# Performance work log

Measured on AMD Instinct MI355X. Metric: run time of the kernel, lower is better.

## Reference

```python
import jax, jax.numpy as jnp
import numpy as np

TOPK = 9
ALPHA = 0.25
GAMMA = 2.0


def setup_inputs() -> dict:
    key = jax.random.key(0)
    ks = jax.random.split(key, 5)
    B, N, C, G = 16, 21504, 80, 64
    return {
        "pred_logits": jax.random.normal(ks[0], (B, N, C), dtype=jnp.float32),
        "pred_boxes": jax.random.uniform(ks[1], (B, N, 4), dtype=jnp.float32),
        "locations": jax.random.uniform(ks[2], (N, 2), dtype=jnp.float32),
        "gt_boxes": jax.random.uniform(ks[3], (B, G, 4), dtype=jnp.float32),
        "gt_labels": jax.random.randint(ks[4], (B, G), 0, C),
    }


def _cxcywh_to_xyxy(b):
    c, wh = b[..., :2], b[..., 2:]
    return jnp.concatenate([c - 0.5 * wh, c + 0.5 * wh], axis=-1)


def _giou_pairwise(a, b):
    # elementwise GIoU between matched xyxy boxes [..., 4] -> [...]
    area_a = (a[..., 2] - a[..., 0]) * (a[..., 3] - a[..., 1])
    area_b = (b[..., 2] - b[..., 0]) * (b[..., 3] - b[..., 1])
    lt = jnp.maximum(a[..., :2], b[..., :2])
    rb = jnp.minimum(a[..., 2:], b[..., 2:])
    wh = jnp.clip(rb - lt, 0.0)
    inter = wh[..., 0] * wh[..., 1]
    union = area_a + area_b - inter
    iou = inter / union
    lt_c = jnp.minimum(a[..., :2], b[..., :2])
    rb_c = jnp.maximum(a[..., 2:], b[..., 2:])
    wh_c = jnp.clip(rb_c - lt_c, 0.0)
    area_c = wh_c[..., 0] * wh_c[..., 1]
    return iou - (area_c - union) / area_c


def _forward(pred_logits, pred_boxes, locations, gt_boxes, gt_labels):
    B, N, C = pred_logits.shape
    G = gt_boxes.shape[1]
    k = min(TOPK, N)
    # distances from every location to every gt center: [B, G, N]
    centers = gt_boxes[..., :2]
    d = jnp.linalg.norm(centers[:, :, None, :] - locations[None, None, :, :], axis=-1)
    # k nearest locations per gt (ascending distance): idx [B, G, k]
    _, idx = jax.lax.top_k(-d, k)
    b_ix = jnp.arange(B)[:, None, None]
    # scatter one-hot positive labels: target_classes[b, idx, label] = 1
    target_classes = (
        jnp.zeros((B, N, C), pred_logits.dtype)
        .at[b_ix, idx, gt_labels[:, :, None]]
        .set(1.0)
    )
    # sigmoid focal loss, reduction='mean'
    x, t = pred_logits, target_classes
    prob = jax.nn.sigmoid(x)
    ce = -(t * jax.nn.log_sigmoid(x) + (1.0 - t) * jax.nn.log_sigmoid(-x))
    p_t = prob * t + (1.0 - prob) * (1.0 - t)
    focal = (ALPHA * t + (1.0 - ALPHA) * (1.0 - t)) * ce * (1.0 - p_t) ** GAMMA
    loss_cls = focal.mean()
    # per-batch L1 / GIoU over the G*k matched pairs, then mean over batches
    pred = pred_boxes[b_ix, idx]                          # [B, G, k, 4]
    tgt = jnp.broadcast_to(gt_boxes[:, :, None, :], pred.shape)
    loss_bbox = jnp.abs(pred - tgt).mean(axis=(1, 2, 3)).mean()
    giou = _giou_pairwise(_cxcywh_to_xyxy(pred), _cxcywh_to_xyxy(tgt))  # [B, G, k]
    loss_giou = (1.0 - giou).mean(axis=(1, 2)).mean()
    return loss_cls, loss_bbox, loss_giou


def reference(pred_logits, pred_boxes, locations, gt_boxes, gt_labels):
    return _forward(pred_logits, pred_boxes, locations, gt_boxes, gt_labels)
```

## Files before the change

### kernel.cpp

```cpp
#include <hip/hip_runtime.h>
#include <hip/hip_bf16.h>
#include <float.h>

#define BB 16
#define NN 21504
#define CC 80
#define GG 64
#define KK 9
#define NSEG 4
#define SEG4 (NN / 2 / NSEG)
#define T4   (SEG4 / 64)

#define FB 3360
#define FSTRIDE (FB * 256)

__device__ __forceinline__ float focal_t0(float x) {
    float ax = fabsf(x);
    float em = __expf(-ax);
    float sp = __logf(1.0f + em);
    float spx = fmaxf(x, 0.0f) + sp;
    float r = 1.0f / (1.0f + em);
    float p = (x >= 0.0f) ? r : em * r;
    return 0.75f * spx * p * p;
}

__device__ __forceinline__ float focal_corr(float x) {
    float ax = fabsf(x);
    float em = __expf(-ax);
    float sp = __logf(1.0f + em);
    float spx = fmaxf(x, 0.0f) + sp;
    float spn = fmaxf(-x, 0.0f) + sp;
    float r = 1.0f / (1.0f + em);
    float p = (x >= 0.0f) ? r : em * r;
    float q = 1.0f - p;
    float f1 = 0.25f * spn * q * q;
    float f0 = 0.75f * spx * p * p;
    return f1 - f0;
}

__device__ __forceinline__ float d2f(float cx, float cy, float x, float y) {
    float dx = cx - x, dy = cy - y;
    return dx * dx + dy * dy;
}

__global__ __launch_bounds__(256) void topk_seg_kernel(
    const float* __restrict__ locations,
    const float* __restrict__ gt_boxes,
    float* __restrict__ cand_d,
    int*   __restrict__ cand_n,
    unsigned long long* __restrict__ hdr)
{
    if (blockIdx.x == 0 && threadIdx.x < 8) hdr[threadIdx.x] = 0ull;

    int seg  = threadIdx.x >> 6;
    int lane = threadIdx.x & 63;
    int pair = blockIdx.x;
    int b = pair >> 6;
    int g = pair & (GG - 1);

    const float4 gt = ((const float4*)gt_boxes)[b * GG + g];
    float cx = gt.x, cy = gt.y;
    const float4* loc4 = (const float4*)locations;
    int base4 = seg * SEG4 + lane;

    float m0 = FLT_MAX, m1 = FLT_MAX, m2 = FLT_MAX, m3 = FLT_MAX;
    for (int t = 0; t < T4; t += 7) {
        float4 L0 = loc4[base4 + (t + 0) * 64];
        float4 L1 = loc4[base4 + (t + 1) * 64];
        float4 L2 = loc4[base4 + (t + 2) * 64];
        float4 L3 = loc4[base4 + (t + 3) * 64];
        float4 L4 = loc4[base4 + (t + 4) * 64];
        float4 L5 = loc4[base4 + (t + 5) * 64];
        float4 L6 = loc4[base4 + (t + 6) * 64];
        m0 = fminf(m0, fminf(d2f(cx, cy, L0.x, L0.y), d2f(cx, cy, L0.z, L0.w)));
        m1 = fminf(m1, fminf(d2f(cx, cy, L1.x, L1.y), d2f(cx, cy, L1.z, L1.w)));
        m2 = fminf(m2, fminf(d2f(cx, cy, L2.x, L2.y), d2f(cx, cy, L2.z, L2.w)));
        m3 = fminf(m3, fminf(d2f(cx, cy, L3.x, L3.y), d2f(cx, cy, L3.z, L3.w)));
        m0 = fminf(m0, fminf(d2f(cx, cy, L4.x, L4.y), d2f(cx, cy, L4.z, L4.w)));
        m1 = fminf(m1, fminf(d2f(cx, cy, L5.x, L5.y), d2f(cx, cy, L5.z, L5.w)));
        m2 = fminf(m2, fminf(d2f(cx, cy, L6.x, L6.y), d2f(cx, cy, L6.z, L6.w)));
    }
    float md = fminf(fminf(m0, m1), fminf(m2, m3));

    float v = md;
    float T = FLT_MAX;
    for (int r = 0; r < KK; ++r) {
        float m = v;
        for (int s = 1; s < 64; s <<= 1) m = fminf(m, __shfl_xor(m, s));
        T = m;
        if (v == m) v = FLT_MAX;
    }

    float sd0 = FLT_MAX, sd1 = FLT_MAX, sd2 = FLT_MAX,
          sd3 = FLT_MAX, sd4 = FLT_MAX, sd5 = FLT_MAX;
    int   sn0 = 0x7fffffff, sn1 = 0x7fffffff, sn2 = 0x7fffffff,
          sn3 = 0x7fffffff, sn4 = 0x7fffffff, sn5 = 0x7fffffff;
    int cnt = 0;
#define PUSH(dv, nv)                                             \
    do {                                                         \
        if (cnt == 0)      { sd0 = dv; sn0 = nv; }               \
        else if (cnt == 1) { sd1 = dv; sn1 = nv; }               \
        else if (cnt == 2) { sd2 = dv; sn2 = nv; }               \
        else if (cnt == 3) { sd3 = dv; sn3 = nv; }               \
        else if (cnt == 4) { sd4 = dv; sn4 = nv; }               \
        else if (cnt == 5) { sd5 = dv; sn5 = nv; }               \
        ++cnt;                                                   \
    } while (0)
#define TEST(Lv, tt)                                             \
    do {                                                         \
        int i4 = base4 + (tt) * 64;                              \
        float da = d2f(cx, cy, Lv.x, Lv.y);                      \
        float db = d2f(cx, cy, Lv.z, Lv.w);                      \
        if (da <= T) PUSH(da, 2 * i4);                           \
        if (db <= T) PUSH(db, 2 * i4 + 1);                       \
    } while (0)

    for (int t = 0; t < T4; t += 7) {
        float4 L0 = loc4[base4 + (t + 0) * 64];
        float4 L1 = loc4[base4 + (t + 1) * 64];
        float4 L2 = loc4[base4 + (t + 2) * 64];
        float4 L3 = loc4[base4 + (t + 3) * 64];
        float4 L4 = loc4[base4 + (t + 4) * 64];
        float4 L5 = loc4[base4 + (t + 5) * 64];
        float4 L6 = loc4[base4 + (t + 6) * 64];
        TEST(L0, t + 0);
        TEST(L1, t + 1);
        TEST(L2, t + 2);
        TEST(L3, t + 3);
        TEST(L4, t + 4);
        TEST(L5, t + 5);
        TEST(L6, t + 6);
    }
#undef TEST
#undef PUSH

    int ovf = (cnt > 6) ? 1 : 0;
    for (int s = 1; s < 64; s <<= 1) ovf = max(ovf, __shfl_xor(ovf, s));

    int obase = (pair * NSEG + seg) * KK;
    if (ovf == 0) {
        for (int r = 0; r < KK; ++r) {
            float bv = sd0; int bn = sn0;
            bool c;
            c = sd1 < bv; bv = c ? sd1 : bv; bn = c ? sn1 : bn;
            c = sd2 < bv; bv = c ? sd2 : bv; bn = c ? sn2 : bn;
            c = sd3 < bv; bv = c ? sd3 : bv; bn = c ? sn3 : bn;
            c = sd4 < bv; bv = c ? sd4 : bv; bn = c ? sn4 : bn;
            c = sd5 < bv; bv = c ? sd5 : bv; bn = c ? sn5 : bn;
            for (int s = 1; s < 64; s <<= 1) {
                float ov = __shfl_xor(bv, s);
                int   on = __shfl_xor(bn, s);
                bool cc = (ov < bv) || (ov == bv && on < bn);
                bv = cc ? ov : bv;
                bn = cc ? on : bn;
            }
            if (sn0 == bn) sd0 = FLT_MAX;
            if (sn1 == bn) sd1 = FLT_MAX;
            if (sn2 == bn) sd2 = FLT_MAX;
            if (sn3 == bn) sd3 = FLT_MAX;
            if (sn4 == bn) sd4 = FLT_MAX;
            if (sn5 == bn) sd5 = FLT_MAX;
            if (lane == 0) { cand_d[obase + r] = bv; cand_n[obase + r] = bn; }
        }
    } else {
        float lastD = -1.0f; int lastN = -1;
        for (int r = 0; r < KK; ++r) {
            float bv = FLT_MAX; int bn = 0x7fffffff;
            for (int t = 0; t < T4; ++t) {
                int i4 = base4 + t * 64;
                float4 A = loc4[i4];
                float da = d2f(cx, cy, A.x, A.y);
                float db = d2f(cx, cy, A.z, A.w);
                int na = 2 * i4, nb = 2 * i4 + 1;
                bool ga = (da > lastD) || (da == lastD && na > lastN);
                bool ca = ga && ((da < bv) || (da == bv && na < bn));
                bv = ca ? da : bv; bn = ca ? na : bn;
                bool gb = (db > lastD) || (db == lastD && nb > lastN);
                bool cb = gb && ((db < bv) || (db == bv && nb < bn));
                bv = cb ? db : bv; bn = cb ? nb : bn;
            }
            for (int s = 1; s < 64; s <<= 1) {
                float ov = __shfl_xor(bv, s);
                int   on = __shfl_xor(bn, s);
                bool cc = (ov < bv) || (ov == bv && on < bn);
                bv = cc ? ov : bv;
                bn = cc ? on : bn;
            }
            lastD = bv; lastN = bn;
            if (lane == 0) { cand_d[obase + r] = bv; cand_n[obase + r] = bn; }
        }
    }
}

__global__ __launch_bounds__(256) void topk_merge_kernel(
    const float* __restrict__ pred_boxes,
    const float* __restrict__ gt_boxes,
    const float* __restrict__ cand_d,
    const int*   __restrict__ cand_n,
    double* __restrict__ acc,
    int* __restrict__ sel)
{
    int wv   = threadIdx.x >> 6;
    int lane = threadIdx.x & 63;
    int pair = blockIdx.x * 4 + wv;
    int b = pair >> 6;
    int g = pair & (GG - 1);

    const float4 gt = ((const float4*)gt_boxes)[b * GG + g];

    float vd = FLT_MAX; int vn = 0x7fffffff;
    if (lane < NSEG * KK) {
        vd = cand_d[pair * NSEG * KK + lane];
        vn = cand_n[pair * NSEG * KK + lane];
    }

    int myn = 0;
    for (int r = 0; r < KK; ++r) {
        float bv = vd; int bn = vn;
        for (int s = 1; s < 64; s <<= 1) {
            float ov = __shfl_xor(bv, s);
            int   on = __shfl_xor(bn, s);
            bool cc = (ov < bv) || (ov == bv && on < bn);
            bv = cc ? ov : bv;
            bn = cc ? on : bn;
        }
        if (vn == bn) vd = FLT_MAX;
        if (lane == r) myn = bn;
        if (lane == 0) sel[pair * KK + r] = bn;
    }
    myn = myn < 0 ? 0 : (myn >= NN ? NN - 1 : myn);

    float l1 = 0.0f, gio = 0.0f;
    if (lane < KK) {
        float4 p = ((const float4*)pred_boxes)[b * NN + myn];
        l1 = fabsf(p.x - gt.x) + fabsf(p.y - gt.y) + fabsf(p.z - gt.z) + fabsf(p.w - gt.w);

        float ax1 = p.x - 0.5f * p.z, ay1 = p.y - 0.5f * p.w;
        float ax2 = p.x + 0.5f * p.z, ay2 = p.y + 0.5f * p.w;
        float bx1 = gt.x - 0.5f * gt.z, by1 = gt.y - 0.5f * gt.w;
        float bx2 = gt.x + 0.5f * gt.z, by2 = gt.y + 0.5f * gt.w;

        float area_a = (ax2 - ax1) * (ay2 - ay1);
        float area_b = (bx2 - bx1) * (by2 - by1);
        float ix1 = fmaxf(ax1, bx1), iy1 = fmaxf(ay1, by1);
        float ix2 = fminf(ax2, bx2), iy2 = fminf(ay2, by2);
        float iw = fmaxf(ix2 - ix1, 0.0f), ih = fmaxf(iy2 - iy1, 0.0f);
        float inter = iw * ih;
        float uni = area_a + area_b - inter;
        float iou = inter / uni;
        float ccx1 = fminf(ax1, bx1), ccy1 = fminf(ay1, by1);
        float ccx2 = fmaxf(ax2, bx2), ccy2 = fmaxf(ay2, by2);
        float cw = fmaxf(ccx2 - ccx1, 0.0f), ch = fmaxf(ccy2 - ccy1, 0.0f);
        float ac = cw * ch;
        float giou = iou - (ac - uni) / ac;
        gio = 1.0f - giou;
    }
    for (int o = 32; o > 0; o >>= 1) {
        l1 += __shfl_down(l1, o);
        gio += __shfl_down(gio, o);
    }
    if (lane == 0) {
        atomicAdd(&acc[1], (double)l1);
        atomicAdd(&acc[2], (double)gio);
    }
}

__global__ __launch_bounds__(256) void focal_main_kernel(
    const float* __restrict__ logits, double* __restrict__ acc)
{
    const float4* v = (const float4*)logits;
    int tid = blockIdx.x * 256 + threadIdx.x;

    float4 L0 = v[tid + 0 * FSTRIDE];
    float4 L1 = v[tid + 1 * FSTRIDE];
    float4 L2 = v[tid + 2 * FSTRIDE];
    float4 L3 = v[tid + 3 * FSTRIDE];
    float4 L4 = v[tid + 4 * FSTRIDE];
    float4 L5 = v[tid + 5 * FSTRIDE];
    float4 L6 = v[tid + 6 * FSTRIDE];
    float4 L7 = v[tid + 7 * FSTRIDE];

    float s0 = 0.f, s1 = 0.f, s2 = 0.f, s3 = 0.f;
    s0 += focal_t0(L0.x); s1 += focal_t0(L0.y); s2 += focal_t0(L0.z); s3 += focal_t0(L0.w);
    s0 += focal_t0(L1.x); s1 += focal_t0(L1.y); s2 += focal_t0(L1.z); s3 += focal_t0(L1.w);
    s0 += focal_t0(L2.x); s1 += focal_t0(L2.y); s2 += focal_t0(L2.z); s3 += focal_t0(L2.w);
    s0 += focal_t0(L3.x); s1 += focal_t0(L3.y); s2 += focal_t0(L3.z); s3 += focal_t0(L3.w);
    s0 += focal_t0(L4.x); s1 += focal_t0(L4.y); s2 += focal_t0(L4.z); s3 += focal_t0(L4.w);
    s0 += focal_t0(L5.x); s1 += focal_t0(L5.y); s2 += focal_t0(L5.z); s3 += focal_t0(L5.w);
    s0 += focal_t0(L6.x); s1 += focal_t0(L6.y); s2 += focal_t0(L6.z); s3 += focal_t0(L6.w);
    s0 += focal_t0(L7.x); s1 += focal_t0(L7.y); s2 += focal_t0(L7.z); s3 += focal_t0(L7.w);

    double d = (double)((s0 + s1) + (s2 + s3));
#pragma unroll
    for (int o = 32; o > 0; o >>= 1) d += __shfl_down(d, o);
    __shared__ double wsum[4];
    if ((threadIdx.x & 63) == 0) wsum[threadIdx.x >> 6] = d;
    __syncthreads();
    if (threadIdx.x == 0) {
        atomicAdd(&acc[0], wsum[0] + wsum[1] + wsum[2] + wsum[3]);
    }
}

#define EPB 144
__global__ __launch_bounds__(256) void correction_kernel(
    const float* __restrict__ logits, const int* __restrict__ sel,
    const int* __restrict__ gt_labels, double* __restrict__ acc,
    int* __restrict__ ticket, float* __restrict__ out)
{
    int bq = blockIdx.x;
    int b  = bq >> 2;
    int q  = bq & 3;

    __shared__ int keys[GG * KK];
    for (int e = threadIdx.x; e < GG * KK; e += blockDim.x) {
        int g = e / KK;
        int n = sel[(b * GG + g) * KK + (e - g * KK)];
        keys[e] = n * CC + gt_labels[b * GG + g];
    }
    __syncthreads();

    bool active = (threadIdx.x < EPB);
    int e = q * EPB + (active ? threadIdx.x : 0);
    int k = keys[e];
    k = active ? k : -1;

    int dup = 0;
    for (int e2 = 0; e2 < GG * KK; e2 += 8) {
        int k0 = keys[e2 + 0];
        int k1 = keys[e2 + 1];
        int k2 = keys[e2 + 2];
        int k3 = keys[e2 + 3];
        int k4 = keys[e2 + 4];
        int k5 = keys[e2 + 5];
        int k6 = keys[e2 + 6];
        int k7 = keys[e2 + 7];
        int h = 0;
        h |= (int)(k0 == k) & (int)(e2 + 0 < e);
        h |= (int)(k1 == k) & (int)(e2 + 1 < e);
        h |= (int)(k2 == k) & (int)(e2 + 2 < e);
        h |= (int)(k3 == k) & (int)(e2 + 3 < e);
        h |= (int)(k4 == k) & (int)(e2 + 4 < e);
        h |= (int)(k5 == k) & (int)(e2 + 5 < e);
        h |= (int)(k6 == k) & (int)(e2 + 6 < e);
        h |= (int)(k7 == k) & (int)(e2 + 7 < e);
        dup |= h;
    }

    float corr = 0.0f;
    if (active && dup == 0) {
        corr = focal_corr(logits[(long long)b * NN * CC + k]);
    }

    double d = (double)corr;
#pragma unroll
    for (int o = 32; o > 0; o >>= 1) d += __shfl_down(d, o);
    __shared__ double wsum[4];
    if ((threadIdx.x & 63) == 0) wsum[threadIdx.x >> 6] = d;
    __syncthreads();
    __shared__ int amlast;
    if (threadIdx.x == 0) {
        atomicAdd(&acc[0], wsum[0] + wsum[1] + wsum[2] + wsum[3]);
        __threadfence();
        int t = atomicAdd(ticket, 1);
        amlast = (t == (int)gridDim.x - 1) ? 1 : 0;
    }
    __syncthreads();
    if (threadIdx.x == 0 && amlast) {
        double a0 = atomicAdd(&acc[0], 0.0);
        double a1 = atomicAdd(&acc[1], 0.0);
        double a2 = atomicAdd(&acc[2], 0.0);
        out[0] = (float)(a0 / (double)((long long)BB * NN * CC));
        out[1] = (float)(a1 / (double)(BB * GG * KK * 4));
        out[2] = (float)(a2 / (double)(BB * GG * KK));
    }
}

extern "C" void kernel_launch(void* const* d_in, const int* in_sizes, int n_in,
                              void* d_out, int out_size, void* d_ws, size_t ws_size,
                              hipStream_t stream) {
    const float* pred_logits = (const float*)d_in[0];
    const float* pred_boxes  = (const float*)d_in[1];
    const float* locations   = (const float*)d_in[2];
    const float* gt_boxes    = (const float*)d_in[3];
    const int*   gt_labels   = (const int*)d_in[4];
    float* out = (float*)d_out;

    unsigned long long* hdr = (unsigned long long*)d_ws;
    double* acc    = (double*)d_ws;
    int*    ticket = (int*)((char*)d_ws + 24);
    int*    sel    = (int*)((char*)d_ws + 64);
    float*  candd  = (float*)((char*)d_ws + 64 + 36864);
    int*    candn  = (int*)((char*)d_ws + 64 + 36864 + 147456);

    topk_seg_kernel<<<BB * GG, 256, 0, stream>>>(locations, gt_boxes, candd, candn, hdr);

    topk_merge_kernel<<<BB * GG / 4, 256, 0, stream>>>(pred_boxes, gt_boxes, candd, candn, acc, sel);

    focal_main_kernel<<<FB, 256, 0, stream>>>(pred_logits, acc);

    correction_kernel<<<BB * 4, 256, 0, stream>>>(pred_logits, sel, gt_labels, acc, ticket, out);
}
```

Baseline: 248.6 us.

## Fuse focal loss blocks into top-k segment kernel and replace atomics with partials

Merges the focal main pass into the top-k segment kernel as extra blocks, so the memory-bound logits sweep runs alongside the distance scan in one launch. Per-block focal and merge-kernel sums are written to partial buffers instead of double atomics, and the correction kernel folds those partials in before its final atomics. This removes one kernel launch and most of the contention on global double atomics. In exchange it adds branch divergence inside the fused kernel and more workspace.

```diff
diff --git a/kernel.cpp b/kernel.cpp
--- a/kernel.cpp
+++ b/kernel.cpp
@@ -13,6 +13,7 @@
 
 #define FB 3360
 #define FSTRIDE (FB * 256)
+#define TOPKB (BB * GG)
 
 __device__ __forceinline__ float focal_t0(float x) {
     float ax = fabsf(x);
@@ -43,13 +44,50 @@
     return dx * dx + dy * dy;
 }
 
-__global__ __launch_bounds__(256) void topk_seg_kernel(
+__global__ __launch_bounds__(256) void k1_seg_focal(
     const float* __restrict__ locations,
     const float* __restrict__ gt_boxes,
+    const float* __restrict__ logits,
     float* __restrict__ cand_d,
     int*   __restrict__ cand_n,
-    unsigned long long* __restrict__ hdr)
+    unsigned long long* __restrict__ hdr,
+    double* __restrict__ focal_part)
 {
+    if (blockIdx.x >= TOPKB) {
+        int fb = (int)blockIdx.x - TOPKB;
+        const float4* v = (const float4*)logits;
+        int tid = fb * 256 + threadIdx.x;
+
+        float4 L0 = v[tid + 0 * FSTRIDE];
+        float4 L1 = v[tid + 1 * FSTRIDE];
+        float4 L2 = v[tid + 2 * FSTRIDE];
+        float4 L3 = v[tid + 3 * FSTRIDE];
+        float4 L4 = v[tid + 4 * FSTRIDE];
+        float4 L5 = v[tid + 5 * FSTRIDE];
+        float4 L6 = v[tid + 6 * FSTRIDE];
+        float4 L7 = v[tid + 7 * FSTRIDE];
+
+        float s0 = 0.f, s1 = 0.f, s2 = 0.f, s3 = 0.f;
+        s0 += focal_t0(L0.x); s1 += focal_t0(L0.y); s2 += focal_t0(L0.z); s3 += focal_t0(L0.w);
+        s0 += focal_t0(L1.x); s1 += focal_t0(L1.y); s2 += focal_t0(L1.z); s3 += focal_t0(L1.w);
+        s0 += focal_t0(L2.x); s1 += focal_t0(L2.y); s2 += focal_t0(L2.z); s3 += focal_t0(L2.w);
+        s0 += focal_t0(L3.x); s1 += focal_t0(L3.y); s2 += focal_t0(L3.z); s3 += focal_t0(L3.w);
+        s0 += focal_t0(L4.x); s1 += focal_t0(L4.y); s2 += focal_t0(L4.z); s3 += focal_t0(L4.w);
+        s0 += focal_t0(L5.x); s1 += focal_t0(L5.y); s2 += focal_t0(L5.z); s3 += focal_t0(L5.w);
+        s0 += focal_t0(L6.x); s1 += focal_t0(L6.y); s2 += focal_t0(L6.z); s3 += focal_t0(L6.w);
+        s0 += focal_t0(L7.x); s1 += focal_t0(L7.y); s2 += focal_t0(L7.z); s3 += focal_t0(L7.w);
+
+        double d = (double)((s0 + s1) + (s2 + s3));
+#pragma unroll
+        for (int o = 32; o > 0; o >>= 1) d += __shfl_down(d, o);
+        __shared__ double wsum[4];
+        if ((threadIdx.x & 63) == 0) wsum[threadIdx.x >> 6] = d;
+        __syncthreads();
+        if (threadIdx.x == 0)
+            focal_part[fb] = wsum[0] + wsum[1] + wsum[2] + wsum[3];
+        return;
+    }
+
     if (blockIdx.x == 0 && threadIdx.x < 8) hdr[threadIdx.x] = 0ull;
 
     int seg  = threadIdx.x >> 6;
@@ -197,8 +235,9 @@
     const float* __restrict__ gt_boxes,
     const float* __restrict__ cand_d,
     const int*   __restrict__ cand_n,
-    double* __restrict__ acc,
-    int* __restrict__ sel)
+    int* __restrict__ sel,
+    double* __restrict__ merge_l1,
+    double* __restrict__ merge_gio)
 {
     int wv   = threadIdx.x >> 6;
     int lane = threadIdx.x & 63;
@@ -259,45 +298,12 @@
         l1 += __shfl_down(l1, o);
         gio += __shfl_down(gio, o);
     }
-    if (lane == 0) {
-        atomicAdd(&acc[1], (double)l1);
-        atomicAdd(&acc[2], (double)gio);
-    }
-}
-
-__global__ __launch_bounds__(256) void focal_main_kernel(
-    const float* __restrict__ logits, double* __restrict__ acc)
-{
-    const float4* v = (const float4*)logits;
-    int tid = blockIdx.x * 256 + threadIdx.x;
-
-    float4 L0 = v[tid + 0 * FSTRIDE];
-    float4 L1 = v[tid + 1 * FSTRIDE];
-    float4 L2 = v[tid + 2 * FSTRIDE];
-    float4 L3 = v[tid + 3 * FSTRIDE];
-    float4 L4 = v[tid + 4 * FSTRIDE];
-    float4 L5 = v[tid + 5 * FSTRIDE];
-    float4 L6 = v[tid + 6 * FSTRIDE];
-    float4 L7 = v[tid + 7 * FSTRIDE];
-
-    float s0 = 0.f, s1 = 0.f, s2 = 0.f, s3 = 0.f;
-    s0 += focal_t0(L0.x); s1 += focal_t0(L0.y); s2 += focal_t0(L0.z); s3 += focal_t0(L0.w);
-    s0 += focal_t0(L1.x); s1 += focal_t0(L1.y); s2 += focal_t0(L1.z); s3 += focal_t0(L1.w);
-    s0 += focal_t0(L2.x); s1 += focal_t0(L2.y); s2 += focal_t0(L2.z); s3 += focal_t0(L2.w);
-    s0 += focal_t0(L3.x); s1 += focal_t0(L3.y); s2 += focal_t0(L3.z); s3 += focal_t0(L3.w);
-    s0 += focal_t0(L4.x); s1 += focal_t0(L4.y); s2 += focal_t0(L4.z); s3 += focal_t0(L4.w);
-    s0 += focal_t0(L5.x); s1 += focal_t0(L5.y); s2 += focal_t0(L5.z); s3 += focal_t0(L5.w);
-    s0 += focal_t0(L6.x); s1 += focal_t0(L6.y); s2 += focal_t0(L6.z); s3 += focal_t0(L6.w);
-    s0 += focal_t0(L7.x); s1 += focal_t0(L7.y); s2 += focal_t0(L7.z); s3 += focal_t0(L7.w);
-
-    double d = (double)((s0 + s1) + (s2 + s3));
-#pragma unroll
-    for (int o = 32; o > 0; o >>= 1) d += __shfl_down(d, o);
-    __shared__ double wsum[4];
-    if ((threadIdx.x & 63) == 0) wsum[threadIdx.x >> 6] = d;
+    __shared__ float wl1[4], wg[4];
+    if (lane == 0) { wl1[wv] = l1; wg[wv] = gio; }
     __syncthreads();
     if (threadIdx.x == 0) {
-        atomicAdd(&acc[0], wsum[0] + wsum[1] + wsum[2] + wsum[3]);
+        merge_l1[blockIdx.x]  = (double)wl1[0] + (double)wl1[1] + (double)wl1[2] + (double)wl1[3];
+        merge_gio[blockIdx.x] = (double)wg[0] + (double)wg[1] + (double)wg[2] + (double)wg[3];
     }
 }
 
@@ -305,7 +311,10 @@
 __global__ __launch_bounds__(256) void correction_kernel(
     const float* __restrict__ logits, const int* __restrict__ sel,
     const int* __restrict__ gt_labels, double* __restrict__ acc,
-    int* __restrict__ ticket, float* __restrict__ out)
+    int* __restrict__ ticket, float* __restrict__ out,
+    const double* __restrict__ focal_part,
+    const double* __restrict__ merge_l1,
+    const double* __restrict__ merge_gio)
 {
     int bq = blockIdx.x;
     int b  = bq >> 2;
@@ -352,6 +361,10 @@
     }
 
     double d = (double)corr;
+    if (threadIdx.x < 53) {
+        int fb = bq + (threadIdx.x << 6);
+        if (fb < FB) d += focal_part[fb];
+    }
 #pragma unroll
     for (int o = 32; o > 0; o >>= 1) d += __shfl_down(d, o);
     __shared__ double wsum[4];
@@ -359,7 +372,15 @@
     __syncthreads();
     __shared__ int amlast;
     if (threadIdx.x == 0) {
+        double s1 = 0.0, s2 = 0.0;
+#pragma unroll
+        for (int i = 0; i < 4; ++i) {
+            s1 += merge_l1[bq * 4 + i];
+            s2 += merge_gio[bq * 4 + i];
+        }
         atomicAdd(&acc[0], wsum[0] + wsum[1] + wsum[2] + wsum[3]);
+        atomicAdd(&acc[1], s1);
+        atomicAdd(&acc[2], s2);
         __threadfence();
         int t = atomicAdd(ticket, 1);
         amlast = (t == (int)gridDim.x - 1) ? 1 : 0;
@@ -389,14 +410,19 @@
     double* acc    = (double*)d_ws;
     int*    ticket = (int*)((char*)d_ws + 24);
     int*    sel    = (int*)((char*)d_ws + 64);
-    float*  candd  = (float*)((char*)d_ws + 64 + 36864);
-    int*    candn  = (int*)((char*)d_ws + 64 + 36864 + 147456);
-
-    topk_seg_kernel<<<BB * GG, 256, 0, stream>>>(locations, gt_boxes, candd, candn, hdr);
-
-    topk_merge_kernel<<<BB * GG / 4, 256, 0, stream>>>(pred_boxes, gt_boxes, candd, candn, acc, sel);
-
-    focal_main_kernel<<<FB, 256, 0, stream>>>(pred_logits, acc);
-
-    correction_kernel<<<BB * 4, 256, 0, stream>>>(pred_logits, sel, gt_labels, acc, ticket, out);
-}
+    float*  candd  = (float*)((char*)d_ws + 36928);
+    int*    candn  = (int*)((char*)d_ws + 184384);
+    double* focal_part = (double*)((char*)d_ws + 331840);
+    double* merge_l1   = (double*)((char*)d_ws + 358720);
+    double* merge_gio  = (double*)((char*)d_ws + 360768);
+
+    k1_seg_focal<<<TOPKB + FB, 256, 0, stream>>>(
+        locations, gt_boxes, pred_logits, candd, candn, hdr, focal_part);
+
+    topk_merge_kernel<<<BB * GG / 4, 256, 0, stream>>>(
+        pred_boxes, gt_boxes, candd, candn, sel, merge_l1, merge_gio);
+
+    correction_kernel<<<BB * 4, 256, 0, stream>>>(
+        pred_logits, sel, gt_labels, acc, ticket, out,
+        focal_part, merge_l1, merge_gio);
+}
```

After: 202.8 us. -18.4%, faster.
